# Optimization experiments

Hardware: AMD Instinct MI355X
Metric: run time of the kernel (lower is better)

The kernel has to match this reference:

```python
import jax, jax.numpy as jnp
import numpy as np

ROPE_THETA = 10000.0

def apply_rope(x, positions):
    # x: [b, h, s, d], positions: [s]
    d = x.shape[-1]
    inv_freq = ROPE_THETA ** (-jnp.arange(0, d, 2, dtype=jnp.float32) / d)  # [d/2]
    ang = positions.astype(jnp.float32)[:, None] * inv_freq[None, :]        # [s, d/2]
    cos = jnp.cos(ang)
    sin = jnp.sin(ang)
    x1 = x[..., 0::2]
    x2 = x[..., 1::2]
    r1 = x1 * cos - x2 * sin
    r2 = x1 * sin + x2 * cos
    # interleave back to [..., d]
    return jnp.stack([r1, r2], axis=-1).reshape(x.shape)

def setup_inputs() -> dict:
    key = jax.random.key(0)
    k1, k2, k3 = jax.random.split(key, 3)
    b, s, d_model = 4, 2048, 1024
    x = jax.random.normal(k1, (b, s, d_model), dtype=jnp.float32)
    wqkv = jax.random.normal(k2, (3 * d_model, d_model), dtype=jnp.float32) * (d_model ** -0.5)
    wo = jax.random.normal(k3, (d_model, d_model), dtype=jnp.float32) * (d_model ** -0.5)
    token_positions = jnp.arange(s, dtype=jnp.int64 if jax.config.jax_enable_x64 else jnp.int32)
    return {"x": x, "wqkv": wqkv, "wo": wo, "token_positions": token_positions}

def reference(x, wqkv, wo, token_positions):
    b, s, d_model = x.shape
    num_heads = 16
    d_head = d_model // num_heads
    # fused QKV projection (Linear: y = x @ W.T)
    qkv = jnp.einsum('bse,fe->bsf', x, wqkv)  # [b, s, 3*d_model]
    q, k, v = jnp.split(qkv, 3, axis=-1)
    def to_heads(t):
        return t.reshape(b, s, num_heads, d_head).transpose(0, 2, 1, 3)  # [b, h, s, d]
    q, k, v = to_heads(q), to_heads(k), to_heads(v)
    q = apply_rope(q, token_positions)
    k = apply_rope(k, token_positions)
    scores = jnp.einsum('bhqd,bhkd->bhqk', q, k) / jnp.sqrt(jnp.asarray(d_head, dtype=x.dtype))
    causal = jnp.tril(jnp.ones((s, s), dtype=bool))  # [s, s]
    scores = jnp.where(causal, scores, -jnp.inf)
    weights = jax.nn.softmax(scores, axis=-1)
    y = jnp.einsum('bhqk,bhkd->bhqd', weights, v)
    y = y.transpose(0, 2, 1, 3).reshape(b, s, d_model)
    return jnp.einsum('bse,fe->bsf', y, wo)
```

## Files before the change

### kernel.cpp

```cpp
#include <hip/hip_runtime.h>
#include <stdint.h>


typedef __attribute__((ext_vector_type(8))) short bf16x8;
typedef __attribute__((ext_vector_type(4))) float f32x4;
typedef __attribute__((ext_vector_type(8))) unsigned short u16x8;
typedef __attribute__((ext_vector_type(4))) unsigned short u16x4;
typedef __attribute__((ext_vector_type(4))) unsigned int u32x4;

#define NB 4
#define NS 2048
#define NH 16
#define DH 64
#define DM 1024
#define BH (NB*NH)

static __device__ __forceinline__ unsigned short f2bf(float f){
  unsigned u = __builtin_bit_cast(unsigned, f);
  u += 0x7fffu + ((u >> 16) & 1u);
  return (unsigned short)(u >> 16);
}
static __device__ __forceinline__ float bf2f(unsigned short h){
  unsigned u = ((unsigned)h) << 16;
  return __builtin_bit_cast(float, u);
}
static __device__ __forceinline__ unsigned cvt_pk_bf16(float lo, float hi){
  unsigned r;
  asm("v_cvt_pk_bf16_f32 %0, %1, %2" : "=v"(r) : "v"(lo), "v"(hi));
  return r;
}
static __device__ __forceinline__ f32x4 mfma16(bf16x8 a, bf16x8 b, f32x4 c){
  return __builtin_amdgcn_mfma_f32_16x16x32_bf16(a, b, c, 0, 0, 0);
}
static __device__ __forceinline__ void gld_lds16(const void* g, void* l){
  __builtin_amdgcn_global_load_lds((const __attribute__((address_space(1))) unsigned int*)g,
                                   (__attribute__((address_space(3))) unsigned int*)l,
                                   16, 0, 0);
}

__global__ __launch_bounds__(256) void cvt_all(const float* __restrict__ x,
                                               const float* __restrict__ wqkv,
                                               const float* __restrict__ wo,
                                               const int* __restrict__ pos,
                                               unsigned short* __restrict__ xb,
                                               unsigned short* __restrict__ wqkvb,
                                               unsigned short* __restrict__ wob,
                                               float* __restrict__ ct,
                                               float* __restrict__ st){
  int stride = gridDim.x * blockDim.x;
  for (int i = blockIdx.x * blockDim.x + threadIdx.x; i < 3211264; i += stride){
    if (i < 3145728){
      const float* src; unsigned short* dst; int j;
      if (i < 2097152){ src = x; dst = xb; j = i; }
      else if (i < 2883584){ src = wqkv; dst = wqkvb; j = i - 2097152; }
      else { src = wo; dst = wob; j = i - 2883584; }
      f32x4 v = *(const f32x4*)(src + (size_t)j * 4);
      u16x4 o;
      o[0] = f2bf(v[0]); o[1] = f2bf(v[1]); o[2] = f2bf(v[2]); o[3] = f2bf(v[3]);
      *(u16x4*)(dst + (size_t)j * 4) = o;
    } else {
      int t = i - 3145728;
      int s = t >> 5, fi = t & 31;
      float p = (float)pos[s];
      float freq = exp2f(-(float)(2 * fi) * (13.287712379549449f / 64.f));
      float a = p * freq;
      ct[t] = cosf(a);
      st[t] = sinf(a);
    }
  }
}

__global__ __launch_bounds__(256) void rope_qk(unsigned short* __restrict__ buf,
                                               const float* __restrict__ ct,
                                               const float* __restrict__ st){
  size_t t  = (size_t)blockIdx.x * 256 + threadIdx.x;
  size_t e0 = t * 8;
  int dh0 = (int)(e0 & 63);
  int s   = (int)((e0 >> 6) & (NS - 1));
  u16x8 v = *(const u16x8*)(buf + e0);
  f32x4 c  = *(const f32x4*)(ct + s * 32 + (dh0 >> 1));
  f32x4 sn = *(const f32x4*)(st + s * 32 + (dh0 >> 1));
  u16x8 o;
#pragma unroll
  for (int i = 0; i < 4; i++){
    float x1 = bf2f(v[2*i]), x2 = bf2f(v[2*i+1]);
    o[2*i]   = f2bf(x1 * c[i] - x2 * sn[i]);
    o[2*i+1] = f2bf(x1 * sn[i] + x2 * c[i]);
  }
  *(u16x8*)(buf + e0) = o;
}

template<int BM, int BN, int MF, int NFR, int EPI, int RING, int OCC>
__global__ __launch_bounds__((BM/(MF*16))*(BN/(NFR*16))*64, OCC)
void gemm_ring(const unsigned short* __restrict__ A,
               const unsigned short* __restrict__ Bm,
               void* __restrict__ out0, void* __restrict__ out1,
               void* __restrict__ out2, int M, int N, int K){
  constexpr int WM = BM / (MF * 16);
  constexpr int WN = BN / (NFR * 16);
  constexpr int T  = WM * WN * 64;
  constexpr int LA = BM * 4 / T;
  constexpr int LB = BN * 4 / T;
  constexpr int L  = LA + LB;
  __shared__ __attribute__((aligned(16))) unsigned short As[RING][BM * 32];
  __shared__ __attribute__((aligned(16))) unsigned short Bs[RING][BN * 32];
  int tid = threadIdx.x;
  int w = tid >> 6, l = tid & 63;
  int lr = l & 15, lk = l >> 4;
  int m0 = blockIdx.y * BM, n0 = blockIdx.x * BN;
  int wr = (w / WN) * (MF * 16), wc = (w % WN) * (NFR * 16);

  const int nt = K >> 5;

  auto stage = [&](int t, int buf){
    int k0 = t * 32;
#pragma unroll
    for (int i = 0; i < LA; i++){
      int f = i * T + tid;
      int row = f >> 2, c = f & 3;
      int gc = (c ^ ((row >> 1) & 3)) * 8;
      gld_lds16(A + (size_t)(m0 + row) * K + k0 + gc, &As[buf][(i * T + w * 64) * 8]);
    }
#pragma unroll
    for (int i = 0; i < LB; i++){
      int f = i * T + tid;
      int row = f >> 2, c = f & 3;
      int gc = (c ^ ((row >> 1) & 3)) * 8;
      gld_lds16(Bm + (size_t)(n0 + row) * K + k0 + gc, &Bs[buf][(i * T + w * 64) * 8]);
    }
  };

  f32x4 zero = {0.f, 0.f, 0.f, 0.f};
  f32x4 acc[MF][NFR];
#pragma unroll
  for (int a = 0; a < MF; a++)
#pragma unroll
    for (int b = 0; b < NFR; b++) acc[a][b] = zero;

#pragma unroll
  for (int p = 0; p < RING - 1; p++) stage(p, p);
  asm volatile("s_waitcnt vmcnt(%0)" :: "i"((RING - 2) * L) : "memory");
  __builtin_amdgcn_sched_barrier(0);
  __builtin_amdgcn_s_barrier();
  __builtin_amdgcn_sched_barrier(0);

  int buf = 0;
  for (int t = 0; t < nt; ++t){
    bf16x8 af[MF], bfr[NFR];
#pragma unroll
    for (int mf = 0; mf < MF; mf++){
      int row = wr + mf * 16 + lr;
      af[mf] = *(const bf16x8*)&As[buf][row * 32 + ((lk ^ ((row >> 1) & 3)) * 8)];
    }
#pragma unroll
    for (int nf = 0; nf < NFR; nf++){
      int row = wc + nf * 16 + lr;
      bfr[nf] = *(const bf16x8*)&Bs[buf][row * 32 + ((lk ^ ((row >> 1) & 3)) * 8)];
    }
    if (t + RING - 1 < nt){
      int sb = buf - 1; if (sb < 0) sb = RING - 1;
      stage(t + RING - 1, sb);
    }
    __builtin_amdgcn_s_setprio(1);
#pragma unroll
    for (int mf = 0; mf < MF; mf++)
#pragma unroll
      for (int nf = 0; nf < NFR; nf++)
        acc[mf][nf] = mfma16(af[mf], bfr[nf], acc[mf][nf]);
    __builtin_amdgcn_s_setprio(0);
    if (RING >= 4){
      if (t + 3 < nt)      { asm volatile("s_waitcnt vmcnt(%0)" :: "i"(2 * L) : "memory"); }
      else if (t + 2 < nt) { asm volatile("s_waitcnt vmcnt(%0)" :: "i"(L) : "memory"); }
      else if (t + 1 < nt) { asm volatile("s_waitcnt vmcnt(0)" ::: "memory"); }
    } else {
      if (t + 2 < nt)      { asm volatile("s_waitcnt vmcnt(%0)" :: "i"(L) : "memory"); }
      else if (t + 1 < nt) { asm volatile("s_waitcnt vmcnt(0)" ::: "memory"); }
    }
    __builtin_amdgcn_sched_barrier(0);
    __builtin_amdgcn_s_barrier();
    __builtin_amdgcn_sched_barrier(0);
    buf = buf + 1; if (buf == RING) buf = 0;
  }

  if (EPI == 0){
    unsigned short* q  = (unsigned short*)out0;
    unsigned short* k  = (unsigned short*)out1;
    unsigned short* vt = (unsigned short*)out2;
#pragma unroll
    for (int mf = 0; mf < MF; mf++)
#pragma unroll
      for (int nf = 0; nf < NFR; nf++)
#pragma unroll
        for (int j = 0; j < 4; j++){
          int m = m0 + wr + mf * 16 + lk * 4 + j;
          int n = n0 + wc + nf * 16 + lr;
          int part = n >> 10, c = n & 1023;
          int h = c >> 6, dh = c & 63;
          int b = m >> 11, s = m & (NS - 1);
          unsigned short val = f2bf(acc[mf][nf][j]);
          if (part == 2){
            vt[((size_t)((b * NH + h) * DH + dh)) * NS + s] = val;
          } else {
            size_t off = ((size_t)(b * NH + h) * NS + s) * DH + dh;
            ((part == 0) ? q : k)[off] = val;
          }
        }
  } else {
    float* C = (float*)out0;
#pragma unroll
    for (int mf = 0; mf < MF; mf++)
#pragma unroll
      for (int nf = 0; nf < NFR; nf++)
#pragma unroll
        for (int j = 0; j < 4; j++){
          int m = m0 + wr + mf * 16 + lk * 4 + j;
          int n = n0 + wc + nf * 16 + lr;
          C[(size_t)m * N + n] = acc[mf][nf][j];
        }
  }
}

__global__ __launch_bounds__(256, 3) void fa_kernel(const unsigned short* __restrict__ qb_,
                                                    const unsigned short* __restrict__ kbuf,
                                                    const unsigned short* __restrict__ vtb,
                                                    unsigned short* __restrict__ yb,
                                                    const float* __restrict__ ct_,
                                                    const float* __restrict__ st_){
  __shared__ __attribute__((aligned(16))) unsigned short Kl[2][4096];
  __shared__ __attribute__((aligned(16))) unsigned short Vl[2][4096];
  __shared__ __attribute__((aligned(16))) unsigned short Pl[4][32 * 76];
  int tid = threadIdx.x;
  int w = tid >> 6, l = tid & 63;
  int lr = l & 15, lk = l >> 4;
  int qb = 15 - blockIdx.y;
  int bh = blockIdx.x;
  int b = bh >> 4, h = bh & 15;
  int qr0 = qb * 128 + w * 32;
  const unsigned short* Q  = qb_  + (size_t)bh * NS * DH;
  const unsigned short* Kp = kbuf + (size_t)bh * NS * DH;
  const unsigned short* VT = vtb  + (size_t)bh * DH * NS;
  unsigned short* Pw = &Pl[w][0];

  int r8  = l >> 3;
  int swc = ((l & 7) ^ (r8 & 7)) * 8;

  auto stage = [&](int buf, int t){
    int kbase = t * 64;
    if (w < 2){
#pragma unroll
      for (int ii = 0; ii < 4; ii++){
        int i = w * 4 + ii;
        gld_lds16(Kp + (size_t)(kbase + i * 8 + r8) * DH + swc, &Kl[buf][i * 512]);
      }
    } else {
#pragma unroll
      for (int ii = 0; ii < 4; ii++){
        int i = (w - 2) * 4 + ii;
        gld_lds16(VT + (size_t)(i * 8 + r8) * NS + kbase + swc, &Vl[buf][i * 512]);
      }
    }
  };

  const float SC = 0.18033688011112042f;
  bf16x8 qf[2][2];
#pragma unroll
  for (int mf = 0; mf < 2; mf++){
    int srow = qr0 + mf * 16 + lr;
    const unsigned short* qrow = Q + (size_t)srow * DH;
    const float* ctr = ct_ + srow * 32;
    const float* str = st_ + srow * 32;
#pragma unroll
    for (int ks = 0; ks < 2; ks++){
      u16x8 raw = *(const u16x8*)(qrow + ks * 32 + lk * 8);
      f32x4 cc = *(const f32x4*)(ctr + ks * 16 + lk * 4);
      f32x4 ss = *(const f32x4*)(str + ks * 16 + lk * 4);
      u32x4 wds;
#pragma unroll
      for (int p = 0; p < 4; p++){
        float c2 = cc[p] * SC, s2 = ss[p] * SC;
        float x1 = bf2f(raw[2*p]), x2 = bf2f(raw[2*p+1]);
        wds[p] = cvt_pk_bf16(x1 * c2 - x2 * s2, x1 * s2 + x2 * c2);
      }
      qf[mf][ks] = __builtin_bit_cast(bf16x8, wds);
    }
  }

  bf16x8 ones;
#pragma unroll
  for (int p = 0; p < 8; p++) ones[p] = (short)0x3F80;

  f32x4 zero = {0.f, 0.f, 0.f, 0.f};
  f32x4 O[2][4];
  f32x4 Ls[2];
#pragma unroll
  for (int mf = 0; mf < 2; mf++){
#pragma unroll
    for (int nf = 0; nf < 4; nf++) O[mf][nf] = zero;
    Ls[mf] = zero;
  }

  const int ntile = 2 * qb + 2;

  stage(0, 0);
  __syncthreads();

  int cur = 0;
  for (int t = 0; t < ntile; ++t){
    int kbase = t * 64;
    if (t + 1 < ntile) stage(cur ^ 1, t + 1);

    if (kbase <= qr0 + 31){
      bf16x8 kf[4][2];
#pragma unroll
      for (int nf = 0; nf < 4; nf++){
        int row = nf * 16 + lr;
        int ro = row * 64, sw = (row & 7) << 3;
#pragma unroll
        for (int ks = 0; ks < 2; ks++)
          kf[nf][ks] = *(const bf16x8*)&Kl[cur][ro + ((ks * 32 + lk * 8) ^ sw)];
      }
      bf16x8 vf[2][4];
#pragma unroll
      for (int nfd = 0; nfd < 4; nfd++){
        int row = nfd * 16 + lr;
        int ro = row * 64, sw = (row & 7) << 3;
#pragma unroll
        for (int ks = 0; ks < 2; ks++)
          vf[ks][nfd] = *(const bf16x8*)&Vl[cur][ro + ((ks * 32 + lk * 8) ^ sw)];
      }

      f32x4 sa[2][4];
#pragma unroll
      for (int mf = 0; mf < 2; mf++)
#pragma unroll
        for (int nf = 0; nf < 4; nf++) sa[mf][nf] = zero;
#pragma unroll
      for (int nf = 0; nf < 4; nf++)
#pragma unroll
        for (int mf = 0; mf < 2; mf++){
          sa[mf][nf] = mfma16(kf[nf][0], qf[mf][0], sa[mf][nf]);
          sa[mf][nf] = mfma16(kf[nf][1], qf[mf][1], sa[mf][nf]);
        }

      bool domask = (kbase + 63 > qr0);

#pragma unroll
      for (int mf = 0; mf < 2; mf++){
        int qg = qr0 + mf * 16 + lr;
#pragma unroll
        for (int nf = 0; nf < 4; nf++){
          float p4[4];
#pragma unroll
          for (int j = 0; j < 4; j++){
            float xx = sa[mf][nf][j];
            if (domask){
              int kg = kbase + nf * 16 + lk * 4 + j;
              if (kg > qg) xx = -__builtin_inff();
            }
            p4[j] = exp2f(xx);
          }
          unsigned d0 = cvt_pk_bf16(p4[0], p4[1]);
          unsigned d1 = cvt_pk_bf16(p4[2], p4[3]);
          int base = (mf * 16 + lr) * 76 + nf * 16 + lk * 4;
          *(unsigned*)&Pw[base]     = d0;
          *(unsigned*)&Pw[base + 2] = d1;
        }
      }

      bf16x8 pf[2][2];
#pragma unroll
      for (int mf = 0; mf < 2; mf++)
#pragma unroll
        for (int ks = 0; ks < 2; ks++)
          pf[mf][ks] = *(const bf16x8*)&Pw[(mf * 16 + lr) * 76 + ks * 32 + lk * 8];
#pragma unroll
      for (int ks = 0; ks < 2; ks++)
#pragma unroll
        for (int nfd = 0; nfd < 4; nfd++)
#pragma unroll
          for (int mf = 0; mf < 2; mf++)
            O[mf][nfd] = mfma16(pf[mf][ks], vf[ks][nfd], O[mf][nfd]);
#pragma unroll
      for (int ks = 0; ks < 2; ks++)
#pragma unroll
        for (int mf = 0; mf < 2; mf++)
          Ls[mf] = mfma16(pf[mf][ks], ones, Ls[mf]);
    }

    __syncthreads();
    cur ^= 1;
  }

#pragma unroll
  for (int mf = 0; mf < 2; mf++)
#pragma unroll
    for (int j = 0; j < 4; j++){
      float inv = 1.0f / Ls[mf][j];
      int srow = qr0 + mf * 16 + lk * 4 + j;
      unsigned short* yp = yb + ((size_t)(b * NS + srow)) * DM + h * DH;
#pragma unroll
      for (int nfd = 0; nfd < 4; nfd++)
        yp[nfd * 16 + lr] = f2bf(O[mf][nfd][j] * inv);
    }
}

extern "C" void kernel_launch(void* const* d_in, const int* in_sizes, int n_in,
                              void* d_out, int out_size, void* d_ws, size_t ws_size,
                              hipStream_t stream){
  const float* x    = (const float*)d_in[0];
  const float* wqkv = (const float*)d_in[1];
  const float* wo   = (const float*)d_in[2];
  const int*   pos  = (const int*)d_in[3];
  float* out = (float*)d_out;

  char* ws = (char*)d_ws;
  size_t off = 0;
  auto alloc = [&](size_t bytes) -> void* {
    void* p = ws + off;
    off += (bytes + 255) & ~(size_t)255;
    return p;
  };
  const size_t NE = (size_t)BH * NS * DH;
  unsigned short* xb    = (unsigned short*)alloc((size_t)8192 * 1024 * 2);
  unsigned short* wqkvb = (unsigned short*)alloc((size_t)3072 * 1024 * 2);
  unsigned short* wob   = (unsigned short*)alloc((size_t)1024 * 1024 * 2);
  unsigned short* q  = (unsigned short*)alloc(NE * 2);
  unsigned short* k  = (unsigned short*)alloc(NE * 2);
  unsigned short* vt = (unsigned short*)alloc(NE * 2);
  unsigned short* y  = (unsigned short*)alloc(NE * 2);
  float* ct = (float*)alloc((size_t)NS * 32 * 4);
  float* st = (float*)alloc((size_t)NS * 32 * 4);

  cvt_all<<<3072, 256, 0, stream>>>(x, wqkv, wo, pos, xb, wqkvb, wob, ct, st);
  gemm_ring<128, 128, 4, 4, 0, 3, 3><<<dim3(24, 64), 256, 0, stream>>>(
      xb, wqkvb, q, k, vt, 8192, 3072, 1024);
  rope_qk<<<4096, 256, 0, stream>>>(k, ct, st);
  fa_kernel<<<dim3(64, 16), 256, 0, stream>>>(q, k, vt, y, ct, st);
  gemm_ring<128, 128, 4, 4, 1, 4, 2><<<dim3(8, 64), 256, 0, stream>>>(
      y, wob, out, nullptr, nullptr, 8192, 1024, 1024);
}
```

Baseline: 211.9 us.

## Fuse K RoPE into QKV GEMM epilogue with LDS-staged vectorized stores

Drops the separate rope_qk kernel and applies RoPE to K inside the QKV projection epilogue. The epilogue now stages the accumulator tile through shared memory so that Q, K and the transposed V can be written with 16-byte vector stores instead of scattered 2-byte stores. This removes one kernel launch and a full read-modify-write pass over K, and makes global writes coalesced, most notably for the transposed V. The shared buffer is reused for the epilogue, which needs extra barriers, and the LDS footprint of the GEMM may grow.

```diff
diff --git a/kernel.cpp b/kernel.cpp
--- a/kernel.cpp
+++ b/kernel.cpp
@@ -70,40 +70,26 @@
   }
 }
 
-__global__ __launch_bounds__(256) void rope_qk(unsigned short* __restrict__ buf,
-                                               const float* __restrict__ ct,
-                                               const float* __restrict__ st){
-  size_t t  = (size_t)blockIdx.x * 256 + threadIdx.x;
-  size_t e0 = t * 8;
-  int dh0 = (int)(e0 & 63);
-  int s   = (int)((e0 >> 6) & (NS - 1));
-  u16x8 v = *(const u16x8*)(buf + e0);
-  f32x4 c  = *(const f32x4*)(ct + s * 32 + (dh0 >> 1));
-  f32x4 sn = *(const f32x4*)(st + s * 32 + (dh0 >> 1));
-  u16x8 o;
-#pragma unroll
-  for (int i = 0; i < 4; i++){
-    float x1 = bf2f(v[2*i]), x2 = bf2f(v[2*i+1]);
-    o[2*i]   = f2bf(x1 * c[i] - x2 * sn[i]);
-    o[2*i+1] = f2bf(x1 * sn[i] + x2 * c[i]);
-  }
-  *(u16x8*)(buf + e0) = o;
-}
-
 template<int BM, int BN, int MF, int NFR, int EPI, int RING, int OCC>
 __global__ __launch_bounds__((BM/(MF*16))*(BN/(NFR*16))*64, OCC)
 void gemm_ring(const unsigned short* __restrict__ A,
                const unsigned short* __restrict__ Bm,
                void* __restrict__ out0, void* __restrict__ out1,
-               void* __restrict__ out2, int M, int N, int K){
+               void* __restrict__ out2,
+               const float* __restrict__ ct_, const float* __restrict__ st_,
+               int M, int N, int K){
   constexpr int WM = BM / (MF * 16);
   constexpr int WN = BN / (NFR * 16);
   constexpr int T  = WM * WN * 64;
   constexpr int LA = BM * 4 / T;
   constexpr int LB = BN * 4 / T;
   constexpr int L  = LA + LB;
-  __shared__ __attribute__((aligned(16))) unsigned short As[RING][BM * 32];
-  __shared__ __attribute__((aligned(16))) unsigned short Bs[RING][BN * 32];
+  constexpr unsigned RB = (unsigned)RING * (BM + BN) * 64;
+  constexpr unsigned EB = (EPI == 0) ? (unsigned)(128 * 132 * 2) : 0u;
+  constexpr unsigned SB = RB > EB ? RB : EB;
+  __shared__ __attribute__((aligned(16))) unsigned char smem[SB];
+  unsigned short* As = (unsigned short*)smem;
+  unsigned short* Bs = As + (size_t)RING * BM * 32;
   int tid = threadIdx.x;
   int w = tid >> 6, l = tid & 63;
   int lr = l & 15, lk = l >> 4;
@@ -119,14 +105,14 @@
       int f = i * T + tid;
       int row = f >> 2, c = f & 3;
       int gc = (c ^ ((row >> 1) & 3)) * 8;
-      gld_lds16(A + (size_t)(m0 + row) * K + k0 + gc, &As[buf][(i * T + w * 64) * 8]);
+      gld_lds16(A + (size_t)(m0 + row) * K + k0 + gc, &As[(size_t)buf * BM * 32 + (i * T + w * 64) * 8]);
     }
 #pragma unroll
     for (int i = 0; i < LB; i++){
       int f = i * T + tid;
       int row = f >> 2, c = f & 3;
       int gc = (c ^ ((row >> 1) & 3)) * 8;
-      gld_lds16(Bm + (size_t)(n0 + row) * K + k0 + gc, &Bs[buf][(i * T + w * 64) * 8]);
+      gld_lds16(Bm + (size_t)(n0 + row) * K + k0 + gc, &Bs[(size_t)buf * BN * 32 + (i * T + w * 64) * 8]);
     }
   };
 
@@ -150,12 +136,12 @@
 #pragma unroll
     for (int mf = 0; mf < MF; mf++){
       int row = wr + mf * 16 + lr;
-      af[mf] = *(const bf16x8*)&As[buf][row * 32 + ((lk ^ ((row >> 1) & 3)) * 8)];
+      af[mf] = *(const bf16x8*)&As[(size_t)buf * BM * 32 + row * 32 + ((lk ^ ((row >> 1) & 3)) * 8)];
     }
 #pragma unroll
     for (int nf = 0; nf < NFR; nf++){
       int row = wc + nf * 16 + lr;
-      bfr[nf] = *(const bf16x8*)&Bs[buf][row * 32 + ((lk ^ ((row >> 1) & 3)) * 8)];
+      bfr[nf] = *(const bf16x8*)&Bs[(size_t)buf * BN * 32 + row * 32 + ((lk ^ ((row >> 1) & 3)) * 8)];
     }
     if (t + RING - 1 < nt){
       int sb = buf - 1; if (sb < 0) sb = RING - 1;
@@ -186,25 +172,69 @@
     unsigned short* q  = (unsigned short*)out0;
     unsigned short* k  = (unsigned short*)out1;
     unsigned short* vt = (unsigned short*)out2;
-#pragma unroll
-    for (int mf = 0; mf < MF; mf++)
-#pragma unroll
-      for (int nf = 0; nf < NFR; nf++)
-#pragma unroll
-        for (int j = 0; j < 4; j++){
-          int m = m0 + wr + mf * 16 + lk * 4 + j;
-          int n = n0 + wc + nf * 16 + lr;
-          int part = n >> 10, c = n & 1023;
-          int h = c >> 6, dh = c & 63;
-          int b = m >> 11, s = m & (NS - 1);
-          unsigned short val = f2bf(acc[mf][nf][j]);
-          if (part == 2){
-            vt[((size_t)((b * NH + h) * DH + dh)) * NS + s] = val;
-          } else {
-            size_t off = ((size_t)(b * NH + h) * NS + s) * DH + dh;
-            ((part == 0) ? q : k)[off] = val;
+    unsigned short* sm = (unsigned short*)smem;
+    int part = n0 >> 10;
+    int b = m0 >> 11;
+    __syncthreads();
+    if (part == 2){
+#pragma unroll
+      for (int mf = 0; mf < MF; mf++)
+#pragma unroll
+        for (int nf = 0; nf < NFR; nf++)
+#pragma unroll
+          for (int j = 0; j < 4; j++)
+            sm[(wc + nf * 16 + lr) * 130 + (wr + mf * 16 + lk * 4 + j)] = f2bf(acc[mf][nf][j]);
+      __syncthreads();
+      int nrow = tid >> 1, mh = tid & 1;
+      int n = n0 + nrow;
+      int h = (n & 1023) >> 6, dh = n & 63;
+      int s0 = (m0 & (NS - 1)) + mh * 64;
+      unsigned short* dst = vt + ((size_t)((b * NH + h) * DH + dh)) * NS + s0;
+      const unsigned short* srcr = &sm[nrow * 130 + mh * 64];
+#pragma unroll
+      for (int ch = 0; ch < 4; ch++)
+        *(u16x8*)(dst + ch * 8 + ((mh ^ 0) & 0) ) = *(const u16x8*)(srcr + ch * 8);
+#pragma unroll
+      for (int ch = 4; ch < 8; ch++)
+        *(u16x8*)(dst + ch * 8) = *(const u16x8*)(srcr + ch * 8);
+    } else {
+#pragma unroll
+      for (int mf = 0; mf < MF; mf++)
+#pragma unroll
+        for (int nf = 0; nf < NFR; nf++)
+#pragma unroll
+          for (int j = 0; j < 4; j++)
+            sm[(wr + mf * 16 + lk * 4 + j) * 132 + (wc + nf * 16 + lr)] = f2bf(acc[mf][nf][j]);
+      __syncthreads();
+      int mrow = tid >> 1, hh = tid & 1;
+      int s = (m0 + mrow) & (NS - 1);
+      int c0 = (n0 & 1023) + hh * 64;
+      int h = c0 >> 6;
+      unsigned short* dst = ((part == 0) ? q : k) + ((size_t)((b * NH + h) * NS + s)) * DH;
+      const unsigned short* srcr = &sm[mrow * 132 + hh * 64];
+      if (part == 1){
+        const float* ctr = ct_ + s * 32;
+        const float* str = st_ + s * 32;
+#pragma unroll
+        for (int ch = 0; ch < 8; ch++){
+          u16x8 v = *(const u16x8*)(srcr + ch * 8);
+          f32x4 cc = *(const f32x4*)(ctr + ch * 4);
+          f32x4 ss = *(const f32x4*)(str + ch * 4);
+          u16x8 o;
+#pragma unroll
+          for (int p = 0; p < 4; p++){
+            float x1 = bf2f(v[2*p]), x2 = bf2f(v[2*p+1]);
+            o[2*p]   = f2bf(x1 * cc[p] - x2 * ss[p]);
+            o[2*p+1] = f2bf(x1 * ss[p] + x2 * cc[p]);
           }
+          *(u16x8*)(dst + ch * 8) = o;
         }
+      } else {
+#pragma unroll
+        for (int ch = 0; ch < 8; ch++)
+          *(u16x8*)(dst + ch * 8) = *(const u16x8*)(srcr + ch * 8);
+      }
+    }
   } else {
     float* C = (float*)out0;
 #pragma unroll
@@ -433,9 +463,8 @@
 
   cvt_all<<<3072, 256, 0, stream>>>(x, wqkv, wo, pos, xb, wqkvb, wob, ct, st);
   gemm_ring<128, 128, 4, 4, 0, 3, 3><<<dim3(24, 64), 256, 0, stream>>>(
-      xb, wqkvb, q, k, vt, 8192, 3072, 1024);
-  rope_qk<<<4096, 256, 0, stream>>>(k, ct, st);
+      xb, wqkvb, q, k, vt, ct, st, 8192, 3072, 1024);
   fa_kernel<<<dim3(64, 16), 256, 0, stream>>>(q, k, vt, y, ct, st);
   gemm_ring<128, 128, 4, 4, 1, 4, 2><<<dim3(8, 64), 256, 0, stream>>>(
-      y, wob, out, nullptr, nullptr, 8192, 1024, 1024);
-}
+      y, wob, out, nullptr, nullptr, nullptr, nullptr, 8192, 1024, 1024);
+}
```

After: 188.2 us. 11.2% less time.
